# Kernel optimization log

Hardware: AMD Instinct MI355X
Metric: run time of the kernel (lower is better)

The kernel has to match this reference:

```python
import jax, jax.numpy as jnp
import numpy as np

B, S, D = 8, 2048, 256


def setup_inputs() -> dict:
    key = jax.random.key(0)
    kq, kk, kv, km = jax.random.split(key, 4)
    q = jax.random.normal(kq, (B, S, D), dtype=jnp.float32)
    k = jax.random.normal(kk, (B, S, D), dtype=jnp.float32)
    v = jax.random.normal(kv, (B, S, D), dtype=jnp.float32)
    mask = jax.random.randint(km, (B, S, S), 0, 2, dtype=jnp.int32)
    return {"q": q, "k": k, "v": v, "mask": mask}


def reference(q, k, v, mask):
    d_k = q.shape[-1]
    scale = 1.0 / jnp.sqrt(jnp.float32(d_k))
    # scores: [B, S, S]
    attn = jnp.einsum('bqd,bkd->bqk', q, k) * scale
    attn = jnp.where(mask == 0, jnp.float32(-1e9), attn)
    attn = jax.nn.softmax(attn, axis=-1)
    out = jnp.einsum('bqk,bkd->bqd', attn, v)
    return (out, attn)
```

## Files before the change

### kernel.cpp

```cpp
#include <hip/hip_runtime.h>

constexpr int B = 8, S = 2048, D = 256;
constexpr int TQ = 32;
constexpr float SCALE = 0.0625f;
constexpr int PSTRIDE = 2056;

typedef __attribute__((ext_vector_type(8))) short bf16x8;
typedef __attribute__((ext_vector_type(4))) float f32x4;

__device__ __forceinline__ short f2bf(float f) {
    union { float f; unsigned u; } c; c.f = f;
    unsigned u = c.u + 0x7fffu + ((c.u >> 16) & 1u);
    return (short)(u >> 16);
}

__global__ void conv_bf16(const float* __restrict__ in, short* __restrict__ out, int n4) {
    int i = blockIdx.x * blockDim.x + threadIdx.x;
    if (i < n4) {
        float4 v = ((const float4*)in)[i];
        short4 o; o.x = f2bf(v.x); o.y = f2bf(v.y); o.z = f2bf(v.z); o.w = f2bf(v.w);
        ((short4*)out)[i] = o;
    }
}

__global__ void transpose_v(const float* __restrict__ v, short* __restrict__ vt) {
    const int b = blockIdx.z;
    const int d0 = blockIdx.x * 64, k0 = blockIdx.y * 64;
    const int t = threadIdx.x;
    const int tr = t >> 4, tc = t & 15;
    __shared__ float tile[64][65];
    const float* vb = v + (size_t)b * S * D;
    #pragma unroll
    for (int r = 0; r < 4; ++r) {
        int key = r * 16 + tr;
        float4 x = *(const float4*)(vb + (size_t)(k0 + key) * D + d0 + tc * 4);
        tile[key][tc * 4 + 0] = x.x; tile[key][tc * 4 + 1] = x.y;
        tile[key][tc * 4 + 2] = x.z; tile[key][tc * 4 + 3] = x.w;
    }
    __syncthreads();
    short* vtb = vt + (size_t)b * D * S;
    #pragma unroll
    for (int r = 0; r < 4; ++r) {
        int d = r * 16 + tr;
        short4 o;
        o.x = f2bf(tile[tc * 4 + 0][d]); o.y = f2bf(tile[tc * 4 + 1][d]);
        o.z = f2bf(tile[tc * 4 + 2][d]); o.w = f2bf(tile[tc * 4 + 3][d]);
        *(short4*)(vtb + (size_t)(d0 + d) * S + k0 + tc * 4) = o;
    }
}

__global__ void pack_mask(const int* __restrict__ mask, unsigned short* __restrict__ pm) {
    int t = blockIdx.x * blockDim.x + threadIdx.x;
    int l16 = t & 15;
    int g = (t >> 4) & 7;
    int rowlin = t >> 7;
    const int* mb = mask + (size_t)rowlin * S + g * 256 + l16;
    unsigned v = 0;
    #pragma unroll
    for (int nt = 0; nt < 16; ++nt)
        v |= (mb[(size_t)nt * 16] != 0 ? 1u : 0u) << nt;
    pm[t] = (unsigned short)v;
}

__global__ __launch_bounds__(512, 2) void attn_mfma(
    const short* __restrict__ qb, const short* __restrict__ kb,
    const short* __restrict__ vtb, const unsigned short* __restrict__ pmg,
    float* __restrict__ outg, float* __restrict__ attng)
{
    const int b = blockIdx.y;
    const int i0 = blockIdx.x * TQ;
    const int tid = threadIdx.x;
    const int wave = tid >> 6, lane = tid & 63;
    const int quad = lane >> 4, l16 = lane & 15;

    __shared__ short p_lds[TQ][PSTRIDE];
    __shared__ float red[8][TQ];

    unsigned pmv[2][4];
    {
        const unsigned short* pmb = pmg + (((size_t)b * S + i0 + quad * 4) * 8 + wave) * 16 + l16;
        #pragma unroll
        for (int mt = 0; mt < 2; ++mt)
            #pragma unroll
            for (int r = 0; r < 4; ++r)
                pmv[mt][r] = pmb[(size_t)(mt * 16 + r) * 128];
    }

    bf16x8 aq[2][8];
    const short* qbase = qb + ((size_t)b * S + i0) * D;
    #pragma unroll
    for (int mt = 0; mt < 2; ++mt)
        #pragma unroll
        for (int ks = 0; ks < 8; ++ks)
            aq[mt][ks] = *(const bf16x8*)(qbase + (size_t)(mt * 16 + l16) * D + ks * 32 + quad * 8);

    f32x4 acc[2][16];
    #pragma unroll
    for (int mt = 0; mt < 2; ++mt)
        #pragma unroll
        for (int nt = 0; nt < 16; ++nt)
            acc[mt][nt] = f32x4{0.f, 0.f, 0.f, 0.f};

    const short* kbase = kb + (size_t)b * S * D;
    #pragma unroll
    for (int nt = 0; nt < 16; ++nt) {
        const int n0 = wave * 256 + nt * 16;
        bf16x8 bk[8];
        #pragma unroll
        for (int ks = 0; ks < 8; ++ks)
            bk[ks] = *(const bf16x8*)(kbase + (size_t)(n0 + l16) * D + ks * 32 + quad * 8);
        #pragma unroll
        for (int ks = 0; ks < 8; ++ks) {
            acc[0][nt] = __builtin_amdgcn_mfma_f32_16x16x32_bf16(aq[0][ks], bk[ks], acc[0][nt], 0, 0, 0);
            acc[1][nt] = __builtin_amdgcn_mfma_f32_16x16x32_bf16(aq[1][ks], bk[ks], acc[1][nt], 0, 0, 0);
        }
    }

    float rsum[2][4];
    #pragma unroll
    for (int mt = 0; mt < 2; ++mt)
        #pragma unroll
        for (int r = 0; r < 4; ++r) rsum[mt][r] = 0.f;

    #pragma unroll
    for (int mt = 0; mt < 2; ++mt) {
        #pragma unroll
        for (int nt = 0; nt < 16; ++nt) {
            #pragma unroll
            for (int r = 0; r < 4; ++r) {
                float s = acc[mt][nt][r] * SCALE;
                float sv = ((pmv[mt][r] >> nt) & 1u) ? s : -1e9f;
                float e = __expf(sv);
                acc[mt][nt][r] = e;
                rsum[mt][r] += e;
            }
        }
    }
    #pragma unroll
    for (int mt = 0; mt < 2; ++mt)
        #pragma unroll
        for (int r = 0; r < 4; ++r) {
            float v = rsum[mt][r];
            v += __shfl_xor(v, 1); v += __shfl_xor(v, 2);
            v += __shfl_xor(v, 4); v += __shfl_xor(v, 8);
            rsum[mt][r] = v;
            if (l16 == 0) red[wave][mt * 16 + quad * 4 + r] = v;
        }
    __syncthreads();

    float inv[2][4];
    #pragma unroll
    for (int mt = 0; mt < 2; ++mt)
        #pragma unroll
        for (int r = 0; r < 4; ++r) {
            float tot = 0.f;
            #pragma unroll
            for (int w = 0; w < 8; ++w) tot += red[w][mt * 16 + quad * 4 + r];
            inv[mt][r] = 1.0f / tot;
        }

    #pragma unroll
    for (int mt = 0; mt < 2; ++mt) {
        float* abase = attng + ((size_t)b * S + i0 + mt * 16 + quad * 4) * S;
        #pragma unroll
        for (int nt = 0; nt < 16; ++nt) {
            const int col = wave * 256 + nt * 16 + l16;
            #pragma unroll
            for (int r = 0; r < 4; ++r) {
                float p = acc[mt][nt][r] * inv[mt][r];
                abase[(size_t)r * S + col] = p;
                p_lds[mt * 16 + quad * 4 + r][col] = f2bf(p);
            }
        }
    }
    __syncthreads();

    f32x4 oacc[2][2];
    #pragma unroll
    for (int mt = 0; mt < 2; ++mt)
        #pragma unroll
        for (int nc = 0; nc < 2; ++nc) oacc[mt][nc] = f32x4{0.f, 0.f, 0.f, 0.f};

    const short* vbase = vtb + (size_t)b * D * S;
    const int nb = wave * 32;
    for (int ks = 0; ks < 64; ++ks) {
        bf16x8 ap[2], bv[2];
        #pragma unroll
        for (int mt = 0; mt < 2; ++mt)
            ap[mt] = *(const bf16x8*)&p_lds[mt * 16 + l16][ks * 32 + quad * 8];
        #pragma unroll
        for (int nc = 0; nc < 2; ++nc)
            bv[nc] = *(const bf16x8*)(vbase + (size_t)(nb + nc * 16 + l16) * S + ks * 32 + quad * 8);
        #pragma unroll
        for (int mt = 0; mt < 2; ++mt)
            #pragma unroll
            for (int nc = 0; nc < 2; ++nc)
                oacc[mt][nc] = __builtin_amdgcn_mfma_f32_16x16x32_bf16(ap[mt], bv[nc], oacc[mt][nc], 0, 0, 0);
    }

    #pragma unroll
    for (int mt = 0; mt < 2; ++mt)
        #pragma unroll
        for (int nc = 0; nc < 2; ++nc)
            #pragma unroll
            for (int r = 0; r < 4; ++r) {
                int row = i0 + mt * 16 + quad * 4 + r;
                int col = nb + nc * 16 + l16;
                outg[((size_t)b * S + row) * D + col] = oacc[mt][nc][r];
            }
}

extern "C" void kernel_launch(void* const* d_in, const int* in_sizes, int n_in,
                              void* d_out, int out_size, void* d_ws, size_t ws_size,
                              hipStream_t stream) {
    const float* q    = (const float*)d_in[0];
    const float* k    = (const float*)d_in[1];
    const float* v    = (const float*)d_in[2];
    const int*   mask = (const int*)d_in[3];
    float* out  = (float*)d_out;
    float* attn = out + (size_t)B * S * D;

    const size_t N = (size_t)B * S * D;
    short* qb  = (short*)d_ws;
    short* kb  = qb + N;
    short* vtb = kb + N;
    unsigned short* pm = (unsigned short*)(vtb + N);

    const int n4 = (int)(N / 4);
    conv_bf16<<<dim3(n4 / 256), 256, 0, stream>>>(q, qb, n4);
    conv_bf16<<<dim3(n4 / 256), 256, 0, stream>>>(k, kb, n4);
    transpose_v<<<dim3(D / 64, S / 64, B), 256, 0, stream>>>(v, vtb);
    pack_mask<<<dim3((B * S * 128) / 256), 256, 0, stream>>>(mask, pm);

    attn_mfma<<<dim3(S / TQ, B), 512, 0, stream>>>(qb, kb, vtb, pm, out, attn);
}
```

Baseline: 413.7 us.

## Merge prepass kernels, coalesce mask packing via ballot, interleave attn stores with PV

Merges the four preprocessing kernels (q/k bf16 conversion, V transpose, mask packing) into one launch with a block-range dispatch. Mask packing now reads rows coalesced and builds bits with wave ballots instead of strided per-thread reads. In the main kernel, the normalized attention probabilities stay in registers and their global stores are spread across the P·V MFMA loop, so the large fp32 attn write overlaps with compute. The cost is register pressure from keeping the probabilities live through the PV loop, and the added control flow in the prepass.

```diff
diff --git a/kernel.cpp b/kernel.cpp
--- a/kernel.cpp
+++ b/kernel.cpp
@@ -14,52 +14,69 @@
     return (short)(u >> 16);
 }
 
-__global__ void conv_bf16(const float* __restrict__ in, short* __restrict__ out, int n4) {
-    int i = blockIdx.x * blockDim.x + threadIdx.x;
-    if (i < n4) {
-        float4 v = ((const float4*)in)[i];
-        short4 o; o.x = f2bf(v.x); o.y = f2bf(v.y); o.z = f2bf(v.z); o.w = f2bf(v.w);
+__global__ __launch_bounds__(256) void prepass(
+    const float* __restrict__ q, const float* __restrict__ k,
+    const float* __restrict__ v, const int* __restrict__ mask,
+    short* __restrict__ qb, short* __restrict__ kb,
+    short* __restrict__ vtb, unsigned short* __restrict__ pm)
+{
+    __shared__ float tile[64][65];
+    const int blk = blockIdx.x;
+    const int tid = threadIdx.x;
+
+    if (blk < 8192) {
+        const float* in = (blk < 4096) ? q : k;
+        short* out = (blk < 4096) ? qb : kb;
+        int i = (blk & 4095) * 256 + tid;
+        float4 x = ((const float4*)in)[i];
+        short4 o; o.x = f2bf(x.x); o.y = f2bf(x.y); o.z = f2bf(x.z); o.w = f2bf(x.w);
         ((short4*)out)[i] = o;
-    }
-}
-
-__global__ void transpose_v(const float* __restrict__ v, short* __restrict__ vt) {
-    const int b = blockIdx.z;
-    const int d0 = blockIdx.x * 64, k0 = blockIdx.y * 64;
-    const int t = threadIdx.x;
-    const int tr = t >> 4, tc = t & 15;
-    __shared__ float tile[64][65];
-    const float* vb = v + (size_t)b * S * D;
-    #pragma unroll
-    for (int r = 0; r < 4; ++r) {
-        int key = r * 16 + tr;
-        float4 x = *(const float4*)(vb + (size_t)(k0 + key) * D + d0 + tc * 4);
-        tile[key][tc * 4 + 0] = x.x; tile[key][tc * 4 + 1] = x.y;
-        tile[key][tc * 4 + 2] = x.z; tile[key][tc * 4 + 3] = x.w;
-    }
-    __syncthreads();
-    short* vtb = vt + (size_t)b * D * S;
-    #pragma unroll
-    for (int r = 0; r < 4; ++r) {
-        int d = r * 16 + tr;
-        short4 o;
-        o.x = f2bf(tile[tc * 4 + 0][d]); o.y = f2bf(tile[tc * 4 + 1][d]);
-        o.z = f2bf(tile[tc * 4 + 2][d]); o.w = f2bf(tile[tc * 4 + 3][d]);
-        *(short4*)(vtb + (size_t)(d0 + d) * S + k0 + tc * 4) = o;
-    }
-}
-
-__global__ void pack_mask(const int* __restrict__ mask, unsigned short* __restrict__ pm) {
-    int t = blockIdx.x * blockDim.x + threadIdx.x;
-    int l16 = t & 15;
-    int g = (t >> 4) & 7;
-    int rowlin = t >> 7;
-    const int* mb = mask + (size_t)rowlin * S + g * 256 + l16;
-    unsigned v = 0;
-    #pragma unroll
-    for (int nt = 0; nt < 16; ++nt)
-        v |= (mb[(size_t)nt * 16] != 0 ? 1u : 0u) << nt;
-    pm[t] = (unsigned short)v;
+    } else if (blk < 9216) {
+        int blk2 = blk - 8192;
+        int b = blk2 >> 7, rem = blk2 & 127;
+        int d0 = (rem & 3) * 64, k0 = (rem >> 2) * 64;
+        int tr = tid >> 4, tc = tid & 15;
+        const float* vb = v + (size_t)b * S * D;
+        #pragma unroll
+        for (int r = 0; r < 4; ++r) {
+            int key = r * 16 + tr;
+            float4 x = *(const float4*)(vb + (size_t)(k0 + key) * D + d0 + tc * 4);
+            tile[key][tc * 4 + 0] = x.x; tile[key][tc * 4 + 1] = x.y;
+            tile[key][tc * 4 + 2] = x.z; tile[key][tc * 4 + 3] = x.w;
+        }
+        __syncthreads();
+        short* vtbb = vtb + (size_t)b * D * S;
+        #pragma unroll
+        for (int r = 0; r < 4; ++r) {
+            int d = r * 16 + tr;
+            short4 o;
+            o.x = f2bf(tile[tc * 4 + 0][d]); o.y = f2bf(tile[tc * 4 + 1][d]);
+            o.z = f2bf(tile[tc * 4 + 2][d]); o.w = f2bf(tile[tc * 4 + 3][d]);
+            *(short4*)(vtbb + (size_t)(d0 + d) * S + k0 + tc * 4) = o;
+        }
+    } else {
+        int t2 = blk - 9216;
+        int w = tid >> 6, lane = tid & 63;
+        int l16 = lane & 15;
+        int rowlin = t2 * 4 + w;
+        const int* mrow = mask + (size_t)rowlin * S;
+        unsigned short* pmrow = pm + (size_t)rowlin * 128;
+        #pragma unroll
+        for (int g = 0; g < 8; ++g) {
+            unsigned v16 = 0;
+            #pragma unroll
+            for (int u = 0; u < 4; ++u) {
+                int col = g * 256 + u * 64 + lane;
+                unsigned long long bal = __ballot(mrow[col] != 0);
+                unsigned nib = (unsigned)((bal >> l16) & 1ull)
+                             | (unsigned)((bal >> (l16 + 16)) & 1ull) << 1
+                             | (unsigned)((bal >> (l16 + 32)) & 1ull) << 2
+                             | (unsigned)((bal >> (l16 + 48)) & 1ull) << 3;
+                v16 |= nib << (u * 4);
+            }
+            if (lane < 16) pmrow[g * 16 + l16] = (unsigned short)v16;
+        }
+    }
 }
 
 __global__ __launch_bounds__(512, 2) void attn_mfma(
@@ -161,14 +178,13 @@
 
     #pragma unroll
     for (int mt = 0; mt < 2; ++mt) {
-        float* abase = attng + ((size_t)b * S + i0 + mt * 16 + quad * 4) * S;
         #pragma unroll
         for (int nt = 0; nt < 16; ++nt) {
             const int col = wave * 256 + nt * 16 + l16;
             #pragma unroll
             for (int r = 0; r < 4; ++r) {
                 float p = acc[mt][nt][r] * inv[mt][r];
-                abase[(size_t)r * S + col] = p;
+                acc[mt][nt][r] = p;
                 p_lds[mt * 16 + quad * 4 + r][col] = f2bf(p);
             }
         }
@@ -183,19 +199,32 @@
 
     const short* vbase = vtb + (size_t)b * D * S;
     const int nb = wave * 32;
-    for (int ks = 0; ks < 64; ++ks) {
-        bf16x8 ap[2], bv[2];
-        #pragma unroll
-        for (int mt = 0; mt < 2; ++mt)
-            ap[mt] = *(const bf16x8*)&p_lds[mt * 16 + l16][ks * 32 + quad * 8];
-        #pragma unroll
-        for (int nc = 0; nc < 2; ++nc)
-            bv[nc] = *(const bf16x8*)(vbase + (size_t)(nb + nc * 16 + l16) * S + ks * 32 + quad * 8);
-        #pragma unroll
-        for (int mt = 0; mt < 2; ++mt)
+    float* abase0 = attng + ((size_t)b * S + i0 + quad * 4) * S + wave * 256 + l16;
+
+    #pragma unroll 1
+    for (int kc = 0; kc < 8; ++kc) {
+        #pragma unroll
+        for (int k2 = 0; k2 < 8; ++k2) {
+            const int ks = kc * 8 + k2;
+            bf16x8 ap[2], bv[2];
+            #pragma unroll
+            for (int mt = 0; mt < 2; ++mt)
+                ap[mt] = *(const bf16x8*)&p_lds[mt * 16 + l16][ks * 32 + quad * 8];
             #pragma unroll
             for (int nc = 0; nc < 2; ++nc)
-                oacc[mt][nc] = __builtin_amdgcn_mfma_f32_16x16x32_bf16(ap[mt], bv[nc], oacc[mt][nc], 0, 0, 0);
+                bv[nc] = *(const bf16x8*)(vbase + (size_t)(nb + nc * 16 + l16) * S + ks * 32 + quad * 8);
+            #pragma unroll
+            for (int mt = 0; mt < 2; ++mt)
+                #pragma unroll
+                for (int nc = 0; nc < 2; ++nc)
+                    oacc[mt][nc] = __builtin_amdgcn_mfma_f32_16x16x32_bf16(ap[mt], bv[nc], oacc[mt][nc], 0, 0, 0);
+        }
+        #pragma unroll
+        for (int j = 0; j < 16; ++j) {
+            const int f = kc * 16 + j;
+            const int mt = f >> 6, nt = (f >> 2) & 15, r = f & 3;
+            abase0[(size_t)(mt * 16 + r) * S + nt * 16] = acc[mt][nt][r];
+        }
     }
 
     #pragma unroll
@@ -226,11 +255,6 @@
     short* vtb = kb + N;
     unsigned short* pm = (unsigned short*)(vtb + N);
 
-    const int n4 = (int)(N / 4);
-    conv_bf16<<<dim3(n4 / 256), 256, 0, stream>>>(q, qb, n4);
-    conv_bf16<<<dim3(n4 / 256), 256, 0, stream>>>(k, kb, n4);
-    transpose_v<<<dim3(D / 64, S / 64, B), 256, 0, stream>>>(v, vtb);
-    pack_mask<<<dim3((B * S * 128) / 256), 256, 0, stream>>>(mask, pm);
-
+    prepass<<<dim3(13312), 256, 0, stream>>>(q, k, v, mask, qb, kb, vtb, pm);
     attn_mfma<<<dim3(S / TQ, B), 512, 0, stream>>>(qb, kb, vtb, pm, out, attn);
 }
```

Measured after the change: 467.5 us. +13.0%, slower.
